# Kernel tuning notes

Hardware: AMD Instinct MI355X
Metric: run time of the kernel (lower is better)

## Reference

```python
import jax, jax.numpy as jnp
import numpy as np

D = 384      # d_model
H = 12       # num_heads
DK = 32      # head dim
L = 6        # num_layers
FF = 1536    # FFN intermediate (4*d_model)
EPS = 1e-12  # BERT LayerNorm eps


def layer_norm(x, w, b):
    m = jnp.mean(x, -1, keepdims=True)
    v = jnp.mean((x - m) ** 2, -1, keepdims=True)
    return (x - m) * jax.lax.rsqrt(v + EPS) * w + b


def deltanet(x, mask, Wq, bq, Wk, bk, Wv, bv, Wb, bb, Wg, bg, Wo, bo, fl, sl):
    # Hierarchical delta-rule linear attention with fast/slow decay states.
    B, S, _ = x.shape
    q = (x @ Wq + bq).reshape(B, S, H, DK)
    k = (x @ Wk + bk).reshape(B, S, H, DK)
    k = k / (jnp.linalg.norm(k, axis=-1, keepdims=True) + 1e-6)
    v = (x @ Wv + bv).reshape(B, S, H, DK)
    beta = jax.nn.sigmoid(x @ Wb + bb) * mask[:, :, None]   # [B,S,H] write gate
    g = jax.nn.sigmoid(x @ Wg + bg)                          # [B,S,H] flux mix gate
    af = jax.nn.sigmoid(fl)[None, :, None, None]             # fast decay, init 0.3
    as_ = jax.nn.sigmoid(sl)[None, :, None, None]            # slow decay, init 0.85

    def step(carry, inp):
        Sf, Ss = carry                      # [B,H,DK,DK] states
        qt, kt, vt, bt, gt = inp            # [B,H,DK],[B,H,DK],[B,H,DK],[B,H],[B,H]
        rf = jnp.einsum('bhkd,bhk->bhd', Sf, kt)
        Sf = af * Sf + bt[..., None, None] * kt[..., :, None] * (vt - rf)[:, :, None, :]
        of = jnp.einsum('bhkd,bhk->bhd', Sf, qt)
        rs = jnp.einsum('bhkd,bhk->bhd', Ss, kt)
        Ss = as_ * Ss + bt[..., None, None] * kt[..., :, None] * (vt - rs)[:, :, None, :]
        os_ = jnp.einsum('bhkd,bhk->bhd', Ss, qt)
        out = gt[..., None] * of + (1.0 - gt[..., None]) * os_
        return (Sf, Ss), out

    to_t = lambda a: jnp.moveaxis(a, 1, 0)  # [B,S,...] -> [S,B,...]
    S0 = jnp.zeros((B, H, DK, DK), x.dtype)
    _, out = jax.lax.scan(step, (S0, S0), (to_t(q), to_t(k), to_t(v), to_t(beta), to_t(g)))
    out = jnp.moveaxis(out, 0, 1).reshape(B, S, D)
    return out @ Wo + bo


def _forward(input_ids, attention_mask, word_emb, pos_emb, type_emb, emb_ln_w, emb_ln_b,
             Wq, bq, Wk, bk, Wv, bv, Wbeta, bbeta, Wg, bg, Wo, bo, fast_logit, slow_logit,
             attn_ln_w, attn_ln_b, ffn_w1, ffn_b1, ffn_w2, ffn_b2, ffn_ln_w, ffn_ln_b):
    B, S = input_ids.shape
    mask = attention_mask.astype(jnp.float32)
    x = word_emb[input_ids] + pos_emb[:S][None] + type_emb[0][None, None]
    x = layer_norm(x, emb_ln_w, emb_ln_b)
    for i in range(L):
        res = x
        a = deltanet(x, mask, Wq[i], bq[i], Wk[i], bk[i], Wv[i], bv[i],
                     Wbeta[i], bbeta[i], Wg[i], bg[i], Wo[i], bo[i],
                     fast_logit[i], slow_logit[i])
        x = layer_norm(res + a, attn_ln_w[i], attn_ln_b[i])
        res = x
        h = jax.nn.gelu(x @ ffn_w1[i] + ffn_b1[i], approximate=False)
        x = layer_norm(res + h @ ffn_w2[i] + ffn_b2[i], ffn_ln_w[i], ffn_ln_b[i])
    m = mask[:, :, None]
    emb = jnp.sum(x * m, 1) / jnp.clip(jnp.sum(m, 1), 1e-9)
    return emb / jnp.linalg.norm(emb, axis=1, keepdims=True)


def setup_inputs() -> dict:
    key = jax.random.key(0)
    ks = jax.random.split(key, 16)
    B, S, V, P = 64, 512, 30522, 512
    n = lambda k, shp, s=0.02: jax.random.normal(k, shp, jnp.float32) * s
    return {
        'input_ids': jax.random.randint(ks[0], (B, S), 0, V),
        'attention_mask': jnp.ones((B, S), jnp.int32),
        'word_emb': n(ks[1], (V, D)),
        'pos_emb': n(ks[2], (P, D)),
        'type_emb': n(ks[3], (2, D)),
        'emb_ln_w': jnp.ones((D,)), 'emb_ln_b': jnp.zeros((D,)),
        'Wq': n(ks[4], (L, D, D)), 'bq': jnp.zeros((L, D)),
        'Wk': n(ks[5], (L, D, D)), 'bk': jnp.zeros((L, D)),
        'Wv': n(ks[6], (L, D, D)), 'bv': jnp.zeros((L, D)),
        'Wbeta': n(ks[7], (L, D, H)), 'bbeta': jnp.zeros((L, H)),
        'Wg': n(ks[8], (L, D, H)), 'bg': jnp.zeros((L, H)),
        'Wo': n(ks[9], (L, D, D)), 'bo': jnp.zeros((L, D)),
        'fast_logit': jnp.full((L, H), -0.8473, jnp.float32),  # sigmoid -> 0.3
        'slow_logit': jnp.full((L, H), 1.7346, jnp.float32),   # sigmoid -> 0.85
        'attn_ln_w': jnp.ones((L, D)), 'attn_ln_b': jnp.zeros((L, D)),
        'ffn_w1': n(ks[10], (L, D, FF)), 'ffn_b1': jnp.zeros((L, FF)),
        'ffn_w2': n(ks[11], (L, FF, D)), 'ffn_b2': jnp.zeros((L, D)),
        'ffn_ln_w': jnp.ones((L, D)), 'ffn_ln_b': jnp.zeros((L, D)),
    }


def reference(input_ids, attention_mask, word_emb, pos_emb, type_emb, emb_ln_w, emb_ln_b,
              Wq, bq, Wk, bk, Wv, bv, Wbeta, bbeta, Wg, bg, Wo, bo, fast_logit, slow_logit,
              attn_ln_w, attn_ln_b, ffn_w1, ffn_b1, ffn_w2, ffn_b2, ffn_ln_w, ffn_ln_b):
    return _forward(input_ids, attention_mask, word_emb, pos_emb, type_emb, emb_ln_w, emb_ln_b,
                    Wq, bq, Wk, bk, Wv, bv, Wbeta, bbeta, Wg, bg, Wo, bo, fast_logit, slow_logit,
                    attn_ln_w, attn_ln_b, ffn_w1, ffn_b1, ffn_w2, ffn_b2, ffn_ln_w, ffn_ln_b)
```

## Files before the change

### kernel.cpp

```cpp
#include <hip/hip_runtime.h>
#include <math.h>

#define DD 384
#define HH 12
#define DKK 32
#define LL 6
#define FFF 1536
#define BB 64
#define SS 512
#define MROWS (BB*SS)
#define TB 32
#define LDX 1152

typedef _Float16 f16;
typedef _Float16 half8 __attribute__((ext_vector_type(8)));
typedef float f32x4 __attribute__((ext_vector_type(4)));
typedef float f32x2 __attribute__((ext_vector_type(2)));

__device__ __forceinline__ float sigmoidf_(float x){ return 1.0f/(1.0f+expf(-x)); }

__device__ __forceinline__ float h2f_lo(unsigned int u){
  union { unsigned short s; f16 h; } c; c.s = (unsigned short)(u & 0xffffu); return (float)c.h;
}
__device__ __forceinline__ float h2f_hi(unsigned int u){
  union { unsigned short s; f16 h; } c; c.s = (unsigned short)(u >> 16); return (float)c.h;
}

__device__ __forceinline__ void gl2lds16(const void* g, void* l){
  __builtin_amdgcn_global_load_lds((const __attribute__((address_space(1))) void*)g,
                                   (__attribute__((address_space(3))) void*)l, 16, 0, 0);
}

__global__ __launch_bounds__(256) void embed_ln_kernel(
    const int* __restrict__ ids, const float* __restrict__ we,
    const float* __restrict__ pe, const float* __restrict__ te,
    const float* __restrict__ w, const float* __restrict__ b,
    float* __restrict__ x, f16* __restrict__ xh)
{
  int wv = threadIdx.x >> 6, lane = threadIdx.x & 63;
  int row = blockIdx.x * 4 + wv;
  int s = row & (SS-1);
  int id = ids[row];
  const float* wep = we + (size_t)id * DD;
  const float* pep = pe + (size_t)s * DD;
  float vals[6]; float sum = 0.f;
  #pragma unroll
  for (int i=0;i<6;i++){ int d = lane + 64*i; vals[i] = wep[d] + pep[d] + te[d]; sum += vals[i]; }
  #pragma unroll
  for (int off=32; off>=1; off>>=1) sum += __shfl_xor(sum, off);
  float mean = sum * (1.0f/DD);
  float vs = 0.f;
  #pragma unroll
  for (int i=0;i<6;i++){ float dv = vals[i]-mean; vs += dv*dv; }
  #pragma unroll
  for (int off=32; off>=1; off>>=1) vs += __shfl_xor(vs, off);
  float inv = rsqrtf(vs*(1.0f/DD) + 1e-12f);
  float* xr = x + (size_t)row*DD;
  f16* xhr = xh + (size_t)row*DD;
  #pragma unroll
  for (int i=0;i<6;i++){ int d = lane + 64*i; float o = (vals[i]-mean)*inv*w[d] + b[d]; xr[d]=o; xhr[d]=(f16)o; }
}

__global__ __launch_bounds__(256) void add_ln_kernel(
    float* __restrict__ x, f16* __restrict__ xh, const float* __restrict__ y,
    const float* __restrict__ w, const float* __restrict__ b, int row0)
{
  int wv = threadIdx.x >> 6, lane = threadIdx.x & 63;
  int row = row0 + blockIdx.x * 4 + wv;
  float* xr = x + (size_t)row*DD;
  f16* xhr = xh + (size_t)row*DD;
  const float* yr = y + (size_t)(blockIdx.x*4+wv)*DD;
  float vals[6]; float sum = 0.f;
  #pragma unroll
  for (int i=0;i<6;i++){ int d = lane + 64*i; vals[i] = xr[d] + yr[d]; sum += vals[i]; }
  #pragma unroll
  for (int off=32; off>=1; off>>=1) sum += __shfl_xor(sum, off);
  float mean = sum * (1.0f/DD);
  float vs = 0.f;
  #pragma unroll
  for (int i=0;i<6;i++){ float dv = vals[i]-mean; vs += dv*dv; }
  #pragma unroll
  for (int off=32; off>=1; off>>=1) vs += __shfl_xor(vs, off);
  float inv = rsqrtf(vs*(1.0f/DD) + 1e-12f);
  #pragma unroll
  for (int i=0;i<6;i++){ int d = lane + 64*i; float o = (vals[i]-mean)*inv*w[d] + b[d]; xr[d]=o; xhr[d]=(f16)o; }
}

__global__ __launch_bounds__(256) void biaspack_kernel(
    const float* __restrict__ bq, const float* __restrict__ bk, const float* __restrict__ bv,
    float* __restrict__ dst)
{
  int i = blockIdx.x*256 + threadIdx.x;
  if (i >= LL*LDX) return;
  int l = i / LDX, r = i - l*LDX;
  float v;
  if (r < 384) v = bq[l*DD + r];
  else if (r < 768) v = bk[l*DD + r-384];
  else v = bv[l*DD + r-768];
  dst[i] = v;
}

__global__ __launch_bounds__(256) void wtrans_kernel(
  const float* __restrict__ Wq, const float* __restrict__ Wk, const float* __restrict__ Wv,
  const float* __restrict__ Wo, const float* __restrict__ W1, const float* __restrict__ W2,
  f16* __restrict__ Wt)
{
  __shared__ float T[32][33];
  int bidx = blockIdx.x;
  const float* src; f16* dst; int K, N, tile;
  if (bidx < 576){ int m = bidx/144; tile = bidx - m*144; K=384; N=384;
    src = (m==0)?Wq:(m==1)?Wk:(m==2)?Wv:Wo; dst = Wt + m*147456; }
  else if (bidx < 1152){ tile = bidx-576; K=384; N=1536; src=W1; dst=Wt+589824; }
  else { tile = bidx-1152; K=1536; N=384; src=W2; dst=Wt+1179648; }
  int tN = N>>5;
  int tk = tile / tN, tn = tile - tk*tN;
  int k0 = tk<<5, n0 = tn<<5;
  int r = threadIdx.x >> 3, c4 = (threadIdx.x & 7) << 2;
  float4 vv = *(const float4*)(src + (size_t)(k0+r)*N + n0 + c4);
  T[r][c4+0]=vv.x; T[r][c4+1]=vv.y; T[r][c4+2]=vv.z; T[r][c4+3]=vv.w;
  __syncthreads();
  f16* dp = dst + (size_t)(n0+r)*K + k0 + c4;
  #pragma unroll
  for (int j=0;j<4;j++) dp[j] = (f16)T[c4+j][r];
}

template<int ACT, int OUT16>
__global__ __launch_bounds__(256) void gemm_f16(
    const f16* __restrict__ A, const f16* __restrict__ BT,
    const float* __restrict__ bias, float* __restrict__ Cf, f16* __restrict__ Ch,
    int M, int N, int K, int lda, int ldc)
{
  __shared__ __align__(16) f16 As[128*32];
  __shared__ __align__(16) f16 Bs[128*32];
  int tid = threadIdx.x, lane = tid & 63, wave = tid >> 6;
  int wm = wave >> 1, wn = wave & 1;
  int n0 = blockIdx.x * 128, m0 = blockIdx.y * 128;
  f32x4 acc[4][4] = {};
  int seg0 = wave*2048 + lane*16;
  int ar = lane & 15, kq = (lane >> 4) * 8;

  for (int k0=0; k0<K; k0+=32){
    #pragma unroll
    for (int i=0;i<2;i++){
      int seg = seg0 + i*1024;
      int e = seg >> 1; int row = e >> 5; int kk = e & 31;
      gl2lds16(A  + (size_t)(m0+row)*lda + k0 + kk, (char*)As + seg);
      gl2lds16(BT + (size_t)(n0+row)*K   + k0 + kk, (char*)Bs + seg);
    }
    __syncthreads();
    half8 af[4], bf[4];
    #pragma unroll
    for (int mi=0;mi<4;mi++) af[mi] = *(const half8*)&As[(wm*64 + mi*16 + ar)*32 + kq];
    #pragma unroll
    for (int ni=0;ni<4;ni++) bf[ni] = *(const half8*)&Bs[(wn*64 + ni*16 + ar)*32 + kq];
    #pragma unroll
    for (int mi=0;mi<4;mi++)
      #pragma unroll
      for (int ni=0;ni<4;ni++)
        acc[mi][ni] = __builtin_amdgcn_mfma_f32_16x16x32_f16(af[mi], bf[ni], acc[mi][ni], 0, 0, 0);
    __syncthreads();
  }
  int rb = (lane >> 4) * 4, cb = lane & 15;
  #pragma unroll
  for (int ni=0;ni<4;ni++){
    int cn = n0 + wn*64 + ni*16 + cb;
    float bz = bias[cn];
    #pragma unroll
    for (int mi=0;mi<4;mi++){
      int rm = m0 + wm*64 + mi*16 + rb;
      #pragma unroll
      for (int r=0;r<4;r++){
        float v = acc[mi][ni][r] + bz;
        if (ACT==1) v = 0.5f*v*(1.0f+erff(v*0.70710678118f));
        if (OUT16) Ch[(size_t)(rm+r)*ldc + cn] = (f16)v;
        else       Cf[(size_t)(rm+r)*ldc + cn] = v;
      }
    }
  }
}

__global__ __launch_bounds__(256) void betag_kernel(
    const float* __restrict__ x, const float* __restrict__ Wb, const float* __restrict__ bb,
    const float* __restrict__ Wg, const float* __restrict__ bg,
    const int* __restrict__ mask, float* __restrict__ beta, float* __restrict__ g)
{
  __shared__ float Ws[384*25];
  for (int idx = threadIdx.x; idx < 384*12; idx += 256){
    int k = idx/12, j = idx - k*12;
    Ws[k*25+j]    = Wb[idx];
    Ws[k*25+12+j] = Wg[idx];
  }
  __syncthreads();
  int wv = threadIdx.x>>6, lane = threadIdx.x&63;
  int row = blockIdx.x*4 + wv;
  const float* xr = x + (size_t)row*DD;
  float accb[12], accg[12];
  #pragma unroll
  for (int j=0;j<12;j++){ accb[j]=0.f; accg[j]=0.f; }
  #pragma unroll
  for (int i=0;i<6;i++){
    int k = lane + 64*i;
    float xv = xr[k];
    const float* wr = &Ws[k*25];
    #pragma unroll
    for (int j=0;j<12;j++){ accb[j] += xv*wr[j]; accg[j] += xv*wr[12+j]; }
  }
  #pragma unroll
  for (int j=0;j<12;j++){
    #pragma unroll
    for (int off=32; off>=1; off>>=1){
      accb[j]+=__shfl_xor(accb[j],off);
      accg[j]+=__shfl_xor(accg[j],off);
    }
  }
  if (lane==0){
    float mk = (float)mask[row];
    #pragma unroll
    for (int j=0;j<12;j++){
      beta[(size_t)row*HH + j] = sigmoidf_(accb[j]+bb[j]) * mk;
      g[(size_t)row*HH + j]    = sigmoidf_(accg[j]+bg[j]);
    }
  }
}

__global__ __launch_bounds__(64) void scan_kernel(
  f16* qkv,
  const float* __restrict__ bp, const float* __restrict__ gp,
  const float* __restrict__ flp, const float* __restrict__ slp)
{
  __shared__ float Kf[2][TB][32];
  __shared__ float Qf[2][TB][32];
  __shared__ float Vf[2][TB][32];
  __shared__ float Bg[2][2][TB];
  __shared__ float Of[TB][64];
  int blk = blockIdx.x;
  int b = blk / HH, h = blk - b*HH;
  int lane = threadIdx.x;
  int col = lane & 31;
  float a = sigmoidf_((lane < 32) ? flp[h] : slp[h]);
  f32x2 a2 = {a, a};
  f32x2 S2[16];
  #pragma unroll
  for (int j=0;j<16;j++) S2[j] = (f32x2){0.f,0.f};
  size_t base = ((size_t)b*SS)*LDX + (size_t)h*DKK;
  f16* qb = qkv + base;
  const f16* kb = qkv + base + 384;
  const f16* vb = qkv + base + 768;
  const float* bbp = bp + ((size_t)b*SS)*HH + h;
  const float* gbp = gp + ((size_t)b*SS)*HH + h;

  int st0 = lane >> 2, part = lane & 3;
  uint4 kv[2], qv[2], vv[2]; float bgv;

  #define LOADG(T0) do {                                                       \
    _Pragma("unroll")                                                          \
    for (int r=0;r<2;r++){                                                     \
      int st = (T0) + r*16 + st0;                                              \
      size_t off = (size_t)st*LDX + part*8;                                    \
      kv[r] = *(const uint4*)(kb + off);                                       \
      qv[r] = *(const uint4*)(qb + off);                                       \
      vv[r] = *(const uint4*)(vb + off);                                       \
    }                                                                          \
    int tb_ = (T0) + (lane & 31);                                              \
    bgv = (lane < 32) ? bbp[(size_t)tb_*HH] : gbp[(size_t)tb_*HH];             \
  } while(0)

  #define STAGE(BUF) do {                                                      \
    _Pragma("unroll")                                                          \
    for (int r=0;r<2;r++){                                                     \
      int s = r*16 + st0;                                                      \
      float kf[8], qf[8], vf[8];                                               \
      kf[0]=h2f_lo(kv[r].x); kf[1]=h2f_hi(kv[r].x); kf[2]=h2f_lo(kv[r].y);     \
      kf[3]=h2f_hi(kv[r].y); kf[4]=h2f_lo(kv[r].z); kf[5]=h2f_hi(kv[r].z);     \
      kf[6]=h2f_lo(kv[r].w); kf[7]=h2f_hi(kv[r].w);                            \
      qf[0]=h2f_lo(qv[r].x); qf[1]=h2f_hi(qv[r].x); qf[2]=h2f_lo(qv[r].y);     \
      qf[3]=h2f_hi(qv[r].y); qf[4]=h2f_lo(qv[r].z); qf[5]=h2f_hi(qv[r].z);     \
      qf[6]=h2f_lo(qv[r].w); qf[7]=h2f_hi(qv[r].w);                            \
      vf[0]=h2f_lo(vv[r].x); vf[1]=h2f_hi(vv[r].x); vf[2]=h2f_lo(vv[r].y);     \
      vf[3]=h2f_hi(vv[r].y); vf[4]=h2f_lo(vv[r].z); vf[5]=h2f_hi(vv[r].z);     \
      vf[6]=h2f_lo(vv[r].w); vf[7]=h2f_hi(vv[r].w);                            \
      float ss = 0.f;                                                          \
      _Pragma("unroll")                                                        \
      for (int i=0;i<8;i++) ss += kf[i]*kf[i];                                 \
      ss += __shfl_xor(ss, 1); ss += __shfl_xor(ss, 2);                        \
      float sc = 1.0f/(sqrtf(ss)+1e-6f);                                       \
      float4 t;                                                                \
      t.x=kf[0]*sc; t.y=kf[1]*sc; t.z=kf[2]*sc; t.w=kf[3]*sc;                  \
      *(float4*)&Kf[BUF][s][part*8] = t;                                       \
      t.x=kf[4]*sc; t.y=kf[5]*sc; t.z=kf[6]*sc; t.w=kf[7]*sc;                  \
      *(float4*)&Kf[BUF][s][part*8+4] = t;                                     \
      t.x=qf[0]; t.y=qf[1]; t.z=qf[2]; t.w=qf[3];                              \
      *(float4*)&Qf[BUF][s][part*8] = t;                                       \
      t.x=qf[4]; t.y=qf[5]; t.z=qf[6]; t.w=qf[7];                              \
      *(float4*)&Qf[BUF][s][part*8+4] = t;                                     \
      t.x=vf[0]; t.y=vf[1]; t.z=vf[2]; t.w=vf[3];                              \
      *(float4*)&Vf[BUF][s][part*8] = t;                                       \
      t.x=vf[4]; t.y=vf[5]; t.z=vf[6]; t.w=vf[7];                              \
      *(float4*)&Vf[BUF][s][part*8+4] = t;                                     \
    }                                                                          \
    Bg[BUF][lane>>5][lane&31] = bgv;                                           \
  } while(0)

  #define LDSTEP(BUF,S,KR,QR,VT,BT) do {                                       \
    const float4* k4_ = (const float4*)&Kf[BUF][S][0];                         \
    const float4* q4_ = (const float4*)&Qf[BUF][S][0];                         \
    _Pragma("unroll")                                                          \
    for (int j=0;j<8;j++){ KR[j]=k4_[j]; QR[j]=q4_[j]; }                       \
    VT = Vf[BUF][S][col]; BT = Bg[BUF][0][S];                                  \
  } while(0)

  #define STEP(KR,QR,VT,BT,S) do {                                            \
    const f32x2* k2_ = (const f32x2*)KR;                                       \
    const f32x2* q2_ = (const f32x2*)QR;                                       \
    f32x2 rA={0.f,0.f},rB={0.f,0.f},rC={0.f,0.f},rD={0.f,0.f};                 \
    _Pragma("unroll")                                                          \
    for (int j=0;j<16;j+=4){                                                   \
      rA += S2[j+0]*k2_[j+0]; rB += S2[j+1]*k2_[j+1];                          \
      rC += S2[j+2]*k2_[j+2]; rD += S2[j+3]*k2_[j+3]; }                        \
    f32x2 rr = (rA+rB)+(rC+rD);                                                \
    float rf = rr.x + rr.y;                                                    \
    float c_ = (BT)*((VT) - rf);                                               \
    f32x2 c2 = {c_, c_};                                                       \
    _Pragma("unroll")                                                          \
    for (int j=0;j<16;j++) S2[j] = a2*S2[j] + c2*k2_[j];                       \
    f32x2 oA={0.f,0.f},oB={0.f,0.f},oC={0.f,0.f},oD={0.f,0.f};                 \
    _Pragma("unroll")                                                          \
    for (int j=0;j<16;j+=4){                                                   \
      oA += S2[j+0]*q2_[j+0]; oB += S2[j+1]*q2_[j+1];                          \
      oC += S2[j+2]*q2_[j+2]; oD += S2[j+3]*q2_[j+3]; }                        \
    f32x2 oo = (oA+oB)+(oC+oD);                                                \
    Of[S][lane] = oo.x + oo.y;                                                 \
  } while(0)

  #define COMBINE(BUF,T0) do {                                                 \
    _Pragma("unroll")                                                          \
    for (int i=0;i<16;i++){                                                    \
      int idx = i*64 + lane;                                                   \
      int s_ = idx >> 5, c_ = idx & 31;                                        \
      float fv = Of[s_][c_];                                                   \
      float sv = Of[s_][c_+32];                                                \
      float gv = Bg[BUF][1][s_];                                               \
      qb[(size_t)((T0)+s_)*LDX + c_] = (f16)(gv*fv + (1.0f-gv)*sv);            \
    }                                                                          \
  } while(0)

  LOADG(0);
  STAGE(0);
  __syncthreads();

  float4 kA[8], qA[8], kB[8], qB[8];
  float vA, bA, vB, bB;

  for (int tile=0; tile<SS/TB; tile++){
    int buf = tile & 1;
    if (tile < SS/TB-1) LOADG((tile+1)*TB);
    LDSTEP(buf, 0, kA, qA, vA, bA);
    #pragma unroll
    for (int s=0; s<TB; s+=2){
      if (s+1 < TB) LDSTEP(buf, s+1, kB, qB, vB, bB);
      STEP(kA, qA, vA, bA, s);
      if (s+2 < TB) LDSTEP(buf, s+2, kA, qA, vA, bA);
      STEP(kB, qB, vB, bB, s+1);
    }
    if (tile < SS/TB-1) STAGE(1-buf);
    COMBINE(buf, tile*TB);
    __syncthreads();
  }
  #undef LOADG
  #undef STAGE
  #undef LDSTEP
  #undef STEP
  #undef COMBINE
}

__global__ __launch_bounds__(384) void pool_kernel(
    const float* __restrict__ x, const int* __restrict__ mask, float* __restrict__ out)
{
  __shared__ float red[384];
  __shared__ float tot;
  int b = blockIdx.x, d = threadIdx.x;
  const float* xb = x + (size_t)b*SS*DD;
  const int* mb = mask + b*SS;
  float s=0.f, sm=0.f;
  for (int t=0;t<SS;t++){ float m=(float)mb[t]; s += xb[(size_t)t*DD+d]*m; sm += m; }
  float emb = s / fmaxf(sm, 1e-9f);
  red[d] = emb*emb;
  __syncthreads();
  for (int off=192; off>=3; off>>=1){
    if (d < off) red[d] += red[d+off];
    __syncthreads();
  }
  if (d==0) tot = red[0]+red[1]+red[2];
  __syncthreads();
  out[(size_t)b*DD + d] = emb * rsqrtf(tot);
}

extern "C" void kernel_launch(void* const* d_in, const int* in_sizes, int n_in,
                              void* d_out, int out_size, void* d_ws, size_t ws_size,
                              hipStream_t stream)
{
  const int*   ids  = (const int*)d_in[0];
  const int*   amask= (const int*)d_in[1];
  const float* we   = (const float*)d_in[2];
  const float* pe   = (const float*)d_in[3];
  const float* te   = (const float*)d_in[4];
  const float* elnw = (const float*)d_in[5];
  const float* elnb = (const float*)d_in[6];
  const float* Wq   = (const float*)d_in[7];
  const float* bq   = (const float*)d_in[8];
  const float* Wk   = (const float*)d_in[9];
  const float* bk   = (const float*)d_in[10];
  const float* Wv   = (const float*)d_in[11];
  const float* bv   = (const float*)d_in[12];
  const float* Wb   = (const float*)d_in[13];
  const float* bb   = (const float*)d_in[14];
  const float* Wg   = (const float*)d_in[15];
  const float* bgp  = (const float*)d_in[16];
  const float* Wo   = (const float*)d_in[17];
  const float* bo   = (const float*)d_in[18];
  const float* fl   = (const float*)d_in[19];
  const float* sl   = (const float*)d_in[20];
  const float* alnw = (const float*)d_in[21];
  const float* alnb = (const float*)d_in[22];
  const float* W1   = (const float*)d_in[23];
  const float* b1   = (const float*)d_in[24];
  const float* W2   = (const float*)d_in[25];
  const float* b2   = (const float*)d_in[26];
  const float* flnw = (const float*)d_in[27];
  const float* flnb = (const float*)d_in[28];
  float* out = (float*)d_out;
  float* w = (float*)d_ws;

  float* x    = w;
  f16*  xh   = (f16*)(w + 12582912);
  f16*  qkvh = (f16*)(w + 18874368);
  float* f2   = w + 37748736;
  float* beta = f2;
  float* gbuf = f2 + 393216;
  f16*  wt   = (f16*)(w + 44040192);
  float* bqkv = w + 44924928;
  f16*  hbf  = qkvh;

  embed_ln_kernel<<<MROWS/4, 256, 0, stream>>>(ids, we, pe, te, elnw, elnb, x, xh);
  biaspack_kernel<<<27,256,0,stream>>>(bq, bk, bv, bqkv);

  for (int l=0;l<LL;l++){
    wtrans_kernel<<<1728,256,0,stream>>>(
        Wq + (size_t)l*147456, Wk + (size_t)l*147456, Wv + (size_t)l*147456,
        Wo + (size_t)l*147456, W1 + (size_t)l*589824, W2 + (size_t)l*589824, wt);

    gemm_f16<0,1><<<dim3(9,256),256,0,stream>>>(xh, wt, bqkv + l*LDX, nullptr, qkvh,
                                                MROWS, LDX, DD, DD, LDX);

    betag_kernel<<<MROWS/4,256,0,stream>>>(x, Wb + (size_t)l*DD*HH, bb + l*HH,
                                           Wg + (size_t)l*DD*HH, bgp + l*HH,
                                           amask, beta, gbuf);
    scan_kernel<<<BB*HH,64,0,stream>>>(qkvh, beta, gbuf, fl + l*HH, sl + l*HH);

    for (int c=0;c<2;c++){
      gemm_f16<0,0><<<dim3(3,128),256,0,stream>>>(qkvh + (size_t)c*16384*LDX, wt+442368,
                                                  bo+l*DD, f2, nullptr, 16384, DD, DD, LDX, DD);
      add_ln_kernel<<<4096,256,0,stream>>>(x, xh, f2, alnw+l*DD, alnb+l*DD, c*16384);
    }
    for (int c=0;c<2;c++){
      gemm_f16<1,1><<<dim3(12,128),256,0,stream>>>(xh + (size_t)c*16384*DD, wt+589824,
                                                   b1+l*FFF, nullptr, hbf, 16384, FFF, DD, DD, FFF);
      gemm_f16<0,0><<<dim3(3,128),256,0,stream>>>(hbf, wt+1179648, b2+l*DD, f2, nullptr,
                                                  16384, DD, FFF, FFF, DD);
      add_ln_kernel<<<4096,256,0,stream>>>(x, xh, f2, flnw+l*DD, flnb+l*DD, c*16384);
    }
  }

  pool_kernel<<<BB,384,0,stream>>>(x, amask, out);
}
```

Baseline: 3.645 ms.

## Hoist weight transposes, run Wo GEMM unchunked with f16 output, widen GEMM K-step

The per-layer weight transpose/convert now runs once for all six layers in a single launch, with each layer's f16 weights kept in their own workspace region (the bias buffer moves to make room). The attention output projection now runs over all rows in one launch. It writes f16 into the unused k-columns of the qkv buffer, and a templated add+LayerNorm reads it, replacing two chunked f32 round-trips. The GEMM inner loop loads a 64-wide K slice per barrier pair, which halves the number of syncs but doubles the shared memory per block. Risks are lower occupancy from the larger LDS footprint, precision loss from the f16 intermediate, and overwriting the k values in the qkv buffer, which are no longer needed after the scan.

```diff
diff --git a/kernel.cpp b/kernel.cpp
--- a/kernel.cpp
+++ b/kernel.cpp
@@ -61,18 +61,25 @@
   for (int i=0;i<6;i++){ int d = lane + 64*i; float o = (vals[i]-mean)*inv*w[d] + b[d]; xr[d]=o; xhr[d]=(f16)o; }
 }
 
+template<int YH>
 __global__ __launch_bounds__(256) void add_ln_kernel(
-    float* __restrict__ x, f16* __restrict__ xh, const float* __restrict__ y,
-    const float* __restrict__ w, const float* __restrict__ b, int row0)
+    float* __restrict__ x, f16* __restrict__ xh, const void* __restrict__ yp,
+    const float* __restrict__ w, const float* __restrict__ b, int row0, int ldy)
 {
   int wv = threadIdx.x >> 6, lane = threadIdx.x & 63;
-  int row = row0 + blockIdx.x * 4 + wv;
+  int rrel = blockIdx.x * 4 + wv;
+  int row = row0 + rrel;
   float* xr = x + (size_t)row*DD;
   f16* xhr = xh + (size_t)row*DD;
-  const float* yr = y + (size_t)(blockIdx.x*4+wv)*DD;
   float vals[6]; float sum = 0.f;
   #pragma unroll
-  for (int i=0;i<6;i++){ int d = lane + 64*i; vals[i] = xr[d] + yr[d]; sum += vals[i]; }
+  for (int i=0;i<6;i++){
+    int d = lane + 64*i;
+    float yv;
+    if (YH) yv = (float)((const f16*)yp)[(size_t)rrel*ldy + d];
+    else    yv = ((const float*)yp)[(size_t)rrel*ldy + d];
+    vals[i] = xr[d] + yv; sum += vals[i];
+  }
   #pragma unroll
   for (int off=32; off>=1; off>>=1) sum += __shfl_xor(sum, off);
   float mean = sum * (1.0f/DD);
@@ -106,12 +113,16 @@
   f16* __restrict__ Wt)
 {
   __shared__ float T[32][33];
-  int bidx = blockIdx.x;
+  int l = blockIdx.x / 1728, bidx = blockIdx.x % 1728;
   const float* src; f16* dst; int K, N, tile;
   if (bidx < 576){ int m = bidx/144; tile = bidx - m*144; K=384; N=384;
-    src = (m==0)?Wq:(m==1)?Wk:(m==2)?Wv:Wo; dst = Wt + m*147456; }
-  else if (bidx < 1152){ tile = bidx-576; K=384; N=1536; src=W1; dst=Wt+589824; }
-  else { tile = bidx-1152; K=1536; N=384; src=W2; dst=Wt+1179648; }
+    const float* w4[4] = {Wq + (size_t)l*147456, Wk + (size_t)l*147456,
+                          Wv + (size_t)l*147456, Wo + (size_t)l*147456};
+    src = w4[m]; dst = Wt + (size_t)l*1769472 + m*147456; }
+  else if (bidx < 1152){ tile = bidx-576; K=384; N=1536;
+    src = W1 + (size_t)l*589824; dst = Wt + (size_t)l*1769472 + 589824; }
+  else { tile = bidx-1152; K=1536; N=384;
+    src = W2 + (size_t)l*589824; dst = Wt + (size_t)l*1769472 + 1179648; }
   int tN = N>>5;
   int tk = tile / tN, tn = tile - tk*tN;
   int k0 = tk<<5, n0 = tn<<5;
@@ -130,8 +141,10 @@
     const float* __restrict__ bias, float* __restrict__ Cf, f16* __restrict__ Ch,
     int M, int N, int K, int lda, int ldc)
 {
-  __shared__ __align__(16) f16 As[128*32];
-  __shared__ __align__(16) f16 Bs[128*32];
+  __shared__ __align__(16) f16 As0[128*32];
+  __shared__ __align__(16) f16 As1[128*32];
+  __shared__ __align__(16) f16 Bs0[128*32];
+  __shared__ __align__(16) f16 Bs1[128*32];
   int tid = threadIdx.x, lane = tid & 63, wave = tid >> 6;
   int wm = wave >> 1, wn = wave & 1;
   int n0 = blockIdx.x * 128, m0 = blockIdx.y * 128;
@@ -139,25 +152,43 @@
   int seg0 = wave*2048 + lane*16;
   int ar = lane & 15, kq = (lane >> 4) * 8;
 
-  for (int k0=0; k0<K; k0+=32){
+  for (int k0=0; k0<K; k0+=64){
     #pragma unroll
     for (int i=0;i<2;i++){
       int seg = seg0 + i*1024;
       int e = seg >> 1; int row = e >> 5; int kk = e & 31;
-      gl2lds16(A  + (size_t)(m0+row)*lda + k0 + kk, (char*)As + seg);
-      gl2lds16(BT + (size_t)(n0+row)*K   + k0 + kk, (char*)Bs + seg);
+      const f16* ap = A  + (size_t)(m0+row)*lda + k0 + kk;
+      const f16* bp = BT + (size_t)(n0+row)*K   + k0 + kk;
+      gl2lds16(ap,      (char*)As0 + seg);
+      gl2lds16(ap + 32, (char*)As1 + seg);
+      gl2lds16(bp,      (char*)Bs0 + seg);
+      gl2lds16(bp + 32, (char*)Bs1 + seg);
     }
     __syncthreads();
-    half8 af[4], bf[4];
-    #pragma unroll
-    for (int mi=0;mi<4;mi++) af[mi] = *(const half8*)&As[(wm*64 + mi*16 + ar)*32 + kq];
-    #pragma unroll
-    for (int ni=0;ni<4;ni++) bf[ni] = *(const half8*)&Bs[(wn*64 + ni*16 + ar)*32 + kq];
-    #pragma unroll
-    for (int mi=0;mi<4;mi++)
-      #pragma unroll
-      for (int ni=0;ni<4;ni++)
-        acc[mi][ni] = __builtin_amdgcn_mfma_f32_16x16x32_f16(af[mi], bf[ni], acc[mi][ni], 0, 0, 0);
+    {
+      half8 af[4], bf[4];
+      #pragma unroll
+      for (int mi=0;mi<4;mi++) af[mi] = *(const half8*)&As0[(wm*64 + mi*16 + ar)*32 + kq];
+      #pragma unroll
+      for (int ni=0;ni<4;ni++) bf[ni] = *(const half8*)&Bs0[(wn*64 + ni*16 + ar)*32 + kq];
+      #pragma unroll
+      for (int mi=0;mi<4;mi++)
+        #pragma unroll
+        for (int ni=0;ni<4;ni++)
+          acc[mi][ni] = __builtin_amdgcn_mfma_f32_16x16x32_f16(af[mi], bf[ni], acc[mi][ni], 0, 0, 0);
+    }
+    {
+      half8 af[4], bf[4];
+      #pragma unroll
+      for (int mi=0;mi<4;mi++) af[mi] = *(const half8*)&As1[(wm*64 + mi*16 + ar)*32 + kq];
+      #pragma unroll
+      for (int ni=0;ni<4;ni++) bf[ni] = *(const half8*)&Bs1[(wn*64 + ni*16 + ar)*32 + kq];
+      #pragma unroll
+      for (int mi=0;mi<4;mi++)
+        #pragma unroll
+        for (int ni=0;ni<4;ni++)
+          acc[mi][ni] = __builtin_amdgcn_mfma_f32_16x16x32_f16(af[mi], bf[ni], acc[mi][ni], 0, 0, 0);
+    }
     __syncthreads();
   }
   int rb = (lane >> 4) * 4, cb = lane & 15;
@@ -438,18 +469,17 @@
   float* beta = f2;
   float* gbuf = f2 + 393216;
   f16*  wt   = (f16*)(w + 44040192);
-  float* bqkv = w + 44924928;
+  float* bqkv = w + 49348608;
   f16*  hbf  = qkvh;
 
   embed_ln_kernel<<<MROWS/4, 256, 0, stream>>>(ids, we, pe, te, elnw, elnb, x, xh);
   biaspack_kernel<<<27,256,0,stream>>>(bq, bk, bv, bqkv);
+  wtrans_kernel<<<LL*1728,256,0,stream>>>(Wq, Wk, Wv, Wo, W1, W2, wt);
 
   for (int l=0;l<LL;l++){
-    wtrans_kernel<<<1728,256,0,stream>>>(
-        Wq + (size_t)l*147456, Wk + (size_t)l*147456, Wv + (size_t)l*147456,
-        Wo + (size_t)l*147456, W1 + (size_t)l*589824, W2 + (size_t)l*589824, wt);
-
-    gemm_f16<0,1><<<dim3(9,256),256,0,stream>>>(xh, wt, bqkv + l*LDX, nullptr, qkvh,
+    f16* wl = wt + (size_t)l*1769472;
+
+    gemm_f16<0,1><<<dim3(9,256),256,0,stream>>>(xh, wl, bqkv + l*LDX, nullptr, qkvh,
                                                 MROWS, LDX, DD, DD, LDX);
 
     betag_kernel<<<MROWS/4,256,0,stream>>>(x, Wb + (size_t)l*DD*HH, bb + l*HH,
@@ -457,17 +487,16 @@
                                            amask, beta, gbuf);
     scan_kernel<<<BB*HH,64,0,stream>>>(qkvh, beta, gbuf, fl + l*HH, sl + l*HH);
 
+    gemm_f16<0,1><<<dim3(3,256),256,0,stream>>>(qkvh, wl+442368, bo+l*DD, nullptr,
+                                                qkvh + 384, MROWS, DD, DD, LDX, LDX);
+    add_ln_kernel<1><<<MROWS/4,256,0,stream>>>(x, xh, qkvh + 384, alnw+l*DD, alnb+l*DD, 0, LDX);
+
     for (int c=0;c<2;c++){
-      gemm_f16<0,0><<<dim3(3,128),256,0,stream>>>(qkvh + (size_t)c*16384*LDX, wt+442368,
-                                                  bo+l*DD, f2, nullptr, 16384, DD, DD, LDX, DD);
-      add_ln_kernel<<<4096,256,0,stream>>>(x, xh, f2, alnw+l*DD, alnb+l*DD, c*16384);
-    }
-    for (int c=0;c<2;c++){
-      gemm_f16<1,1><<<dim3(12,128),256,0,stream>>>(xh + (size_t)c*16384*DD, wt+589824,
+      gemm_f16<1,1><<<dim3(12,128),256,0,stream>>>(xh + (size_t)c*16384*DD, wl+589824,
                                                    b1+l*FFF, nullptr, hbf, 16384, FFF, DD, DD, FFF);
-      gemm_f16<0,0><<<dim3(3,128),256,0,stream>>>(hbf, wt+1179648, b2+l*DD, f2, nullptr,
+      gemm_f16<0,0><<<dim3(3,128),256,0,stream>>>(hbf, wl+1179648, b2+l*DD, f2, nullptr,
                                                   16384, DD, FFF, FFF, DD);
-      add_ln_kernel<<<4096,256,0,stream>>>(x, xh, f2, flnw+l*DD, flnb+l*DD, c*16384);
+      add_ln_kernel<0><<<4096,256,0,stream>>>(x, xh, f2, flnw+l*DD, flnb+l*DD, c*16384, DD);
     }
   }
 
```

New measurement: 3.850 ms. 5.6% more time.
